# Performance work log

Measured on AMD Instinct MI355X. Metric: run time of the kernel, lower is better.

Reference implementation:

```python
import jax, jax.numpy as jnp
import numpy as np


def _c(x):
    # [2, ...] real/imag stacked -> complex
    return x[0] + 1j * x[1]


def _ri(z):
    # complex -> [2, ...] real/imag stacked
    return jnp.stack([jnp.real(z), jnp.imag(z)], axis=0).astype(jnp.float32)


_SHAPES = dict(
    VU=(2, 128, 96), UU=(2, 128, 8, 128), WU=(2, 8, 8, 128), GD=(2, 16, 96, 128),
    UD=(2, 16, 8, 128), WD=(2, 8, 8, 128), Z=(2, 16, 96, 128), HU=(2, 128, 16, 128),
    HD=(2, 16, 128, 128), P=(2, 16, 8, 128), GU=(2, 96, 16, 128), F=(2, 128, 8, 128),
    VD=(2, 96, 128), J=(2, 16, 16, 128, 128),
    conv1_w=(12, 18, 2, 2), conv1_b=(12,), conv2_w=(8, 12, 2, 2), conv2_b=(8,),
    conv3_w=(6, 8, 2, 2), conv3_b=(6,), fc1_w=(1000, 864), fc1_b=(1000,),
    fc2_w=(700, 1000), fc2_b=(700,), fc3_w=(192, 700), fc3_b=(192,))


def setup_inputs() -> dict:
    key = jax.random.key(0)
    keys = jax.random.split(key, len(_SHAPES))
    return {n: jax.random.normal(k, s, jnp.float32) * 0.05
            for (n, s), k in zip(_SHAPES.items(), keys)}


def reference(VU, UU, WU, GD, UD, WD, Z, HU, HD, P, GU, F, VD, J,
              conv1_w, conv1_b, conv2_w, conv2_b, conv3_w, conv3_b,
              fc1_w, fc1_b, fc2_w, fc2_b, fc3_w, fc3_b):
    VUc, UUc, WUc, GDc, UDc, WDc, Zc, HUc, HDc, Pc, GUc, Fc, VDc, Jc = map(
        _c, (VU, UU, WU, GD, UD, WD, Z, HU, HD, P, GU, F, VD, J))
    Mf = VUc.shape[1]

    # A1 = sum_k VU^H UU_k WU_k UU_k^H VU  (vectorized over k)
    T1 = jnp.einsum('nm,nuk->muk', jnp.conj(VUc), UUc)            # VU^H UU
    S1 = jnp.einsum('nvk,nf->vfk', jnp.conj(UUc), VUc)            # UU^H VU
    A1 = jnp.einsum('muk,uvk,vfk->mf', T1, WUc, S1)

    # A2 = sum_l GD_l^H UD_l WD_l UD_l^H GD_l
    T2 = jnp.einsum('nml,ndl->mdl', jnp.conj(GDc), UDc)           # GD^H UD
    S2 = jnp.einsum('ndl,nfl->dfl', jnp.conj(UDc), GDc)
    A2 = jnp.einsum('mdl,del,efl->mf', T2, WDc, S2)

    # A3 = sum_l Z_l^H UD_l WD_l UD_l^H Z_l
    T3 = jnp.einsum('nml,ndl->mdl', jnp.conj(Zc), UDc)            # Z^H UD
    S3 = jnp.einsum('ndl,nfl->dfl', jnp.conj(UDc), Zc)
    A3 = jnp.einsum('mdl,del,efl->mf', T3, WDc, S3)

    # B1 = B1_3 - B1_1 @ B1_2
    PPH = jnp.einsum('auk,buk->abk', Pc, jnp.conj(Pc))            # P P^H per k
    B1_1 = jnp.einsum('muk,uvk,nvk->mn', T1, WUc, jnp.conj(UUc))
    B1_2 = jnp.einsum('nak,abk,fbk->nf', HUc, PPH, jnp.conj(GUc))
    B1_3 = jnp.einsum('muk,vuk,avk,fak->mf', T1, jnp.conj(WUc), jnp.conj(Pc), jnp.conj(GUc))
    B1 = B1_3 - B1_1 @ B1_2

    # B2 = B2_3 - B2_1 @ B2_2
    FFH = jnp.einsum('adl,bdl->ab', Fc, jnp.conj(Fc))             # sum_l F F^H
    B2_1 = jnp.einsum('mdl,del,nel,ntl->mt', T2, WDc, jnp.conj(UDc), HDc)
    B2_2 = jnp.einsum('ab,fb->af', FFH, jnp.conj(VDc))
    B2_3 = jnp.einsum('mdl,edl,tel,ft->mf', T2, jnp.conj(WDc), jnp.conj(Fc), jnp.conj(VDc))
    B2 = B2_3 - B2_1 @ B2_2

    # B3 = -sum_{l,k} Z_l^H UD_l WD_l UD_l^H J_{kl} P_k P_k^H GU_k^H
    TL = jnp.einsum('mdl,del,nel->mnl', T3, WDc, jnp.conj(UDc))   # [Mf, N_D, L]
    Q = jnp.einsum('abk,fbk->afk', PPH, jnp.conj(GUc))            # [N_U, Mf, K]
    R = jnp.einsum('nakl,afk->nfl', Jc, Q)                        # sum over k
    B3 = -jnp.einsum('mnl,nfl->mf', TL, R)

    # C1 = C3 = sum_k GU_k P_k P_k^H GU_k^H ;  C2 = sum_l VD F_l F_l^H VD^H
    C1 = jnp.einsum('fak,abk,gbk->fg', GUc, PPH, jnp.conj(GUc))
    C2 = jnp.einsum('fa,ab,gb->fg', VDc, FFH, jnp.conj(VDc))
    C3 = C1

    # Theta_black_box CNN: cat nine [2,Mf,Mf] along channel -> [1,18,Mf,Mf]
    x = jnp.concatenate([_ri(M) for M in (A1, B1, C1, A2, B2, C2, A3, B3, C3)], axis=0)[None]
    for w, b in ((conv1_w, conv1_b), (conv2_w, conv2_b), (conv3_w, conv3_b)):
        x = jax.nn.relu(jax.lax.conv_general_dilated(
            x, w, (2, 2), 'VALID',
            dimension_numbers=('NCHW', 'OIHW', 'NCHW')) + b[None, :, None, None])
    x = x.reshape(-1, 864)
    x = jax.nn.relu(x @ fc1_w.T + fc1_b)
    x = jax.nn.relu(x @ fc2_w.T + fc2_b)
    x = jax.nn.relu(x @ fc3_w.T + fc3_b)
    return x.reshape(2, Mf)
```

## Files before the change

### kernel.cpp

```cpp
#include <hip/hip_runtime.h>

#define DEV __device__ __forceinline__

#define PL_VU 12288
#define PL_UU 131072
#define PL_WU 8192
#define PL_GD 196608
#define PL_UD 16384
#define PL_WD 8192
#define PL_Z  196608
#define PL_HU 262144
#define PL_HD 262144
#define PL_P  16384
#define PL_GU 196608
#define PL_F  131072
#define PL_VD 12288
#define PL_J  4194304

#define SP_T   98304
#define SP_PPH 32768
#define SP_Q   196608
#define SP_H2  262144

#define W_T1   0
#define W_T2   196608
#define W_T3   393216
#define W_PPH  589824
#define W_VF   655360
#define W_M1   851968
#define W_M1C  1048576
#define W_M2   1245184
#define W_M2C  1441792
#define W_M3   1638400
#define W_QT   1835008
#define W_G2   2228224
#define W_H2   2621440
#define W_U2   3145728
#define W_TL   3538944
#define W_N1   3932160
#define W_R    4325376
#define W_MATS 4718592
#define W_B11  4884480
#define W_B12  4909056
#define W_B21  4933632
#define W_B22  4958208
#define W_C1O  4982784
#define W_C2O  5010432
#define W_C3O  5015040
#define W_F1O  5015904
#define W_F2O  5016904

struct Ins {
  const float *VU,*UU,*WU,*GD,*UD,*WD,*Z,*HU,*HD,*P,*GU,*F,*VD,*J;
};

__global__ __launch_bounds__(256) void stageA(Ins in, float* __restrict__ ws) {
  int b = blockIdx.x, tid = threadIdx.x;
  if (b < 384) {
    int idx = b*256 + tid;
    int k = idx & 127, u = (idx >> 7) & 7, m = idx >> 10;
    float ar=0, ai=0;
    for (int n=0;n<128;++n) {
      float vr = in.VU[n*96+m], vi = in.VU[PL_VU+n*96+m];
      int iu = (n*8+u)*128+k;
      float ur = in.UU[iu], ui = in.UU[PL_UU+iu];
      ar += vr*ur + vi*ui; ai += vr*ui - vi*ur;
    }
    ws[W_T1+idx]=ar; ws[W_T1+SP_T+idx]=ai;
  } else if (b < 768) {
    int idx = (b-384)*256 + tid;
    int l = idx & 127, d = (idx >> 7) & 7, m = idx >> 10;
    float ar=0, ai=0;
    for (int n=0;n<16;++n) {
      int ig = (n*96+m)*128+l, iu = (n*8+d)*128+l;
      float gr = in.GD[ig], gi = in.GD[PL_GD+ig];
      float ur = in.UD[iu], ui = in.UD[PL_UD+iu];
      ar += gr*ur + gi*ui; ai += gr*ui - gi*ur;
    }
    ws[W_T2+idx]=ar; ws[W_T2+SP_T+idx]=ai;
  } else if (b < 1152) {
    int idx = (b-768)*256 + tid;
    int l = idx & 127, d = (idx >> 7) & 7, m = idx >> 10;
    float ar=0, ai=0;
    for (int n=0;n<16;++n) {
      int ig = (n*96+m)*128+l, iu = (n*8+d)*128+l;
      float gr = in.Z[ig], gi = in.Z[PL_Z+ig];
      float ur = in.UD[iu], ui = in.UD[PL_UD+iu];
      ar += gr*ur + gi*ui; ai += gr*ui - gi*ur;
    }
    ws[W_T3+idx]=ar; ws[W_T3+SP_T+idx]=ai;
  } else if (b < 1280) {
    int idx = (b-1152)*256 + tid;
    int k = idx & 127, bb = (idx >> 7) & 15, a = idx >> 11;
    float ar=0, ai=0;
    for (int u=0;u<8;++u) {
      int ia = (a*8+u)*128+k, ib = (bb*8+u)*128+k;
      float pr = in.P[ia], pi = in.P[PL_P+ia];
      float qr = in.P[ib], qi = in.P[PL_P+ib];
      ar += pr*qr + pi*qi; ai += pi*qr - pr*qi;
    }
    ws[W_PPH+idx]=ar; ws[W_PPH+SP_PPH+idx]=ai;
  } else {
    int idx = (b-1280)*256 + tid;
    int l = idx & 127, d = (idx >> 7) & 7, f = idx >> 10;
    float ar=0, ai=0;
    for (int a=0;a<128;++a) {
      float vr = in.VD[f*128+a], vi = in.VD[PL_VD+f*128+a];
      int ix = (a*8+d)*128+l;
      float fr = in.F[ix], fi = in.F[PL_F+ix];
      ar += vr*fr - vi*fi; ai += vr*fi + vi*fr;
    }
    ws[W_VF+idx]=ar; ws[W_VF+SP_T+idx]=ai;
  }
}

template<bool CONJA, bool CONJB, bool BENK, int N, int E>
DEV void inner_seg(const float* __restrict__ A, int Apl,
                   const float* __restrict__ B, int Bpl,
                   float* __restrict__ O, int Opl, int idx) {
  int k = idx & 127;
  int n = (idx >> 7) % N;
  int m = idx / (128*N);
  float ar=0, ai=0;
  #pragma unroll
  for (int e=0;e<E;++e) {
    int ia = (m*E+e)*128+k;
    float xr = A[ia], xi = A[Apl+ia];
    if (CONJA) xi = -xi;
    int ib = BENK ? (e*N+n)*128+k : (n*E+e)*128+k;
    float yr = B[ib], yi = B[Bpl+ib];
    if (CONJB) yi = -yi;
    ar += xr*yr - xi*yi; ai += xr*yi + xi*yr;
  }
  O[idx]=ar; O[Opl+idx]=ai;
}

__global__ __launch_bounds__(256) void stageB(Ins in, float* __restrict__ ws) {
  int b = blockIdx.x, tid = threadIdx.x;
  if (b < 384)       inner_seg<false,false,true ,8, 8>(ws+W_T1,SP_T, in.WU,PL_WU, ws+W_M1, SP_T, b*256+tid);
  else if (b < 768)  inner_seg<false,true ,false,8, 8>(ws+W_T1,SP_T, in.WU,PL_WU, ws+W_M1C,SP_T, (b-384)*256+tid);
  else if (b < 1152) inner_seg<false,false,true ,8, 8>(ws+W_T2,SP_T, in.WD,PL_WD, ws+W_M2, SP_T, (b-768)*256+tid);
  else if (b < 1536) inner_seg<false,true ,false,8, 8>(ws+W_T2,SP_T, in.WD,PL_WD, ws+W_M2C,SP_T, (b-1152)*256+tid);
  else if (b < 1920) inner_seg<false,false,true ,8, 8>(ws+W_T3,SP_T, in.WD,PL_WD, ws+W_M3, SP_T, (b-1536)*256+tid);
  else if (b < 2688) inner_seg<true ,false,false,16,16>(in.GU,PL_GU, ws+W_PPH,SP_PPH, ws+W_QT, SP_Q,  (b-1920)*256+tid);
  else if (b < 3456) inner_seg<false,true ,false,16,16>(in.GU,PL_GU, ws+W_PPH,SP_PPH, ws+W_G2, SP_Q,  (b-2688)*256+tid);
  else if (b < 4480) inner_seg<false,true ,false,16,16>(in.HU,PL_HU, ws+W_PPH,SP_PPH, ws+W_H2, SP_H2, (b-3456)*256+tid);
  else {
    int idx = (b-4480)*256 + tid;
    ((float4*)(ws+W_R))[idx] = make_float4(0.f,0.f,0.f,0.f);
  }
}

__global__ __launch_bounds__(256) void stageC(float* __restrict__ ws, Ins in) {
  int b = blockIdx.x, tid = threadIdx.x;
  if (b < 768)        inner_seg<false,true,false,16,8>(ws+W_M2, SP_T, in.UD,PL_UD, ws+W_U2, SP_Q, b*256+tid);
  else if (b < 1536)  inner_seg<false,true,false,16,8>(ws+W_M3, SP_T, in.UD,PL_UD, ws+W_TL, SP_Q, (b-768)*256+tid);
  else                inner_seg<false,true,false,16,8>(ws+W_M1C,SP_T, in.P, PL_P,  ws+W_N1, SP_Q, (b-1536)*256+tid);
}

__global__ __launch_bounds__(256) void kR(Ins in, float* __restrict__ ws) {
  int bid = blockIdx.x;
  int n  = bid >> 5;
  int lq = (bid >> 3) & 3;
  int kc = bid & 7;
  int tid = threadIdx.x;
  int l  = lq*32 + (tid & 31);
  int fs = tid >> 5;
  int k0 = kc*16;
  __shared__ float2 qt[96][16];
  float2 acc[12];
  #pragma unroll
  for (int j=0;j<12;++j) acc[j] = make_float2(0.f,0.f);
  for (int a=0;a<16;++a) {
    __syncthreads();
    for (int t=tid; t<96*16; t+=256) {
      int f = t >> 4, kk = t & 15;
      int qi = (f*16+a)*128 + k0 + kk;
      qt[f][kk] = make_float2(ws[W_QT+qi], ws[W_QT+SP_Q+qi]);
    }
    __syncthreads();
    const float* Jb = in.J + ((n*16+a)*128 + k0)*128 + l;
    #pragma unroll 4
    for (int kk=0;kk<16;++kk) {
      float jr = Jb[kk*128];
      float ji = Jb[PL_J + kk*128];
      #pragma unroll
      for (int j=0;j<12;++j) {
        float2 q = qt[fs*12+j][kk];
        acc[j].x += jr*q.x - ji*q.y;
        acc[j].y += jr*q.y + ji*q.x;
      }
    }
  }
  #pragma unroll
  for (int j=0;j<12;++j) {
    int f = fs*12+j;
    atomicAdd(&ws[W_R + (n*96+f)*128 + l], acc[j].x);
    atomicAdd(&ws[W_R + SP_Q + (n*96+f)*128 + l], acc[j].y);
  }
}

template<bool CONJB, bool OJC>
DEV void outer_tile(const float* __restrict__ A, int Apl,
                    const float* __restrict__ B, int Bpl,
                    float* __restrict__ C, int Cpl,
                    int J, int O, float scale, int tile) {
  __shared__ float As[16][33], Aip[16][33], Bs[16][33], Bip[16][33];
  int tj = J >> 4;
  int ti_ = tile / tj, tj_ = tile % tj;
  int tx = threadIdx.x & 15, ty = threadIdx.x >> 4;
  float ar=0, ai=0;
  int r0 = threadIdx.x >> 5, c = threadIdx.x & 31;
  for (int o=0;o<O;++o) {
    for (int cc=0;cc<128;cc+=32) {
      __syncthreads();
      #pragma unroll
      for (int rr=r0; rr<16; rr+=8) {
        int aidx = ((ti_*16+rr)*O+o)*128+cc+c;
        As[rr][c]=A[aidx]; Aip[rr][c]=A[Apl+aidx];
        int brow = tj_*16+rr;
        int bidx = OJC ? (o*J+brow)*128+cc+c : (brow*O+o)*128+cc+c;
        Bs[rr][c]=B[bidx]; Bip[rr][c]=B[Bpl+bidx];
      }
      __syncthreads();
      #pragma unroll
      for (int q=0;q<32;++q) {
        float xr=As[ty][q], xi=Aip[ty][q];
        float yr=Bs[tx][q], yi=Bip[tx][q];
        if (CONJB) { ar += xr*yr + xi*yi; ai += xi*yr - xr*yi; }
        else       { ar += xr*yr - xi*yi; ai += xr*yi + xi*yr; }
      }
    }
  }
  int i = ti_*16+ty, j = tj_*16+tx;
  C[i*J+j] = scale*ar; C[Cpl+i*J+j] = scale*ai;
}

__global__ __launch_bounds__(256) void stageD(Ins in, float* __restrict__ ws) {
  int b = blockIdx.x;
  if (b < 36)        outer_tile<true ,false>(ws+W_M1, SP_T,  ws+W_T1, SP_T,  ws+W_MATS+0*18432, 9216, 96, 8,  1.f, b);
  else if (b < 72)   outer_tile<true ,false>(ws+W_M2, SP_T,  ws+W_T2, SP_T,  ws+W_MATS+3*18432, 9216, 96, 8,  1.f, b-36);
  else if (b < 108)  outer_tile<true ,false>(ws+W_M3, SP_T,  ws+W_T3, SP_T,  ws+W_MATS+6*18432, 9216, 96, 8,  1.f, b-72);
  else if (b < 144)  outer_tile<true ,false>(ws+W_G2, SP_Q,  in.GU,   PL_GU, ws+W_MATS+2*18432, 9216, 96, 16, 1.f, b-108);
  else if (b < 180)  outer_tile<true ,false>(ws+W_G2, SP_Q,  in.GU,   PL_GU, ws+W_MATS+8*18432, 9216, 96, 16, 1.f, b-144);
  else if (b < 216)  outer_tile<true ,false>(ws+W_VF, SP_T,  ws+W_VF, SP_T,  ws+W_MATS+5*18432, 9216, 96, 8,  1.f, b-180);
  else if (b < 264)  outer_tile<true ,false>(ws+W_M1, SP_T,  in.UU,   PL_UU, ws+W_B11, 12288, 128, 8,  1.f, b-216);
  else if (b < 312)  outer_tile<true ,false>(ws+W_H2, SP_H2, in.GU,   PL_GU, ws+W_B12, 12288,  96, 16, 1.f, b-264);
  else if (b < 348)  outer_tile<true ,false>(ws+W_N1, SP_Q,  in.GU,   PL_GU, ws+W_MATS+1*18432, 9216, 96, 16, 1.f, b-312);
  else if (b < 396)  outer_tile<false,true >(ws+W_U2, SP_Q,  in.HD,   PL_HD, ws+W_B21, 12288, 128, 16, 1.f, b-348);
  else if (b < 444)  outer_tile<true ,false>(in.F,    PL_F,  ws+W_VF, SP_T,  ws+W_B22, 12288,  96, 8,  1.f, b-396);
  else if (b < 480)  outer_tile<true ,false>(ws+W_M2C,SP_T,  ws+W_VF, SP_T,  ws+W_MATS+4*18432, 9216, 96, 8,  1.f, b-444);
  else               outer_tile<false,true >(ws+W_TL, SP_Q,  ws+W_R,  SP_Q,  ws+W_MATS+7*18432, 9216, 96, 16,-1.f, b-480);
}

__global__ __launch_bounds__(256) void stageE(float* __restrict__ ws) {
  int idx = blockIdx.x*256 + threadIdx.x;
  int seg = idx / 9216;
  int t = idx % 9216;
  int m = t / 96, f = t % 96;
  const float* A = ws + (seg ? W_B21 : W_B11);
  const float* B = ws + (seg ? W_B22 : W_B12);
  float* C = ws + W_MATS + (seg ? 4 : 1)*18432;
  float ar = C[t], ai = C[9216+t];
  for (int n=0;n<128;++n) {
    float xr = A[m*128+n], xi = A[12288+m*128+n];
    float yr = B[n*96+f],  yi = B[12288+n*96+f];
    ar -= xr*yr - xi*yi;
    ai -= xr*yi + xi*yr;
  }
  C[t] = ar; C[9216+t] = ai;
}

__global__ __launch_bounds__(256) void convk(const float* __restrict__ x, const float* __restrict__ w,
                      const float* __restrict__ bias, float* __restrict__ out,
                      int IC, int IW, int OC, int OW) {
  int idx = blockIdx.x*256 + threadIdx.x;
  int total = OC*OW*OW;
  if (idx >= total) return;
  int ow = idx % OW, oh = (idx/OW) % OW, oc = idx/(OW*OW);
  float acc = bias[oc];
  const float* wk = w + oc*IC*4;
  for (int ic=0; ic<IC; ++ic) {
    const float* xp = x + ic*IW*IW + (oh*2)*IW + ow*2;
    acc += xp[0]*wk[0] + xp[1]*wk[1] + xp[IW]*wk[2] + xp[IW+1]*wk[3];
    wk += 4;
  }
  out[idx] = fmaxf(acc, 0.f);
}

__global__ __launch_bounds__(256) void fck(const float* __restrict__ W, const float* __restrict__ b,
                    const float* __restrict__ x, float* __restrict__ out,
                    int nout, int nin) {
  int wave = (blockIdx.x*256 + threadIdx.x) >> 6;
  int lane = threadIdx.x & 63;
  if (wave >= nout) return;
  float acc = 0.f;
  const float* Wr = W + (long)wave*nin;
  for (int c = lane; c < nin; c += 64) acc += Wr[c]*x[c];
  #pragma unroll
  for (int off=32; off; off>>=1) acc += __shfl_down(acc, off, 64);
  if (lane==0) out[wave] = fmaxf(acc + b[wave], 0.f);
}

extern "C" void kernel_launch(void* const* d_in, const int* in_sizes, int n_in,
                              void* d_out, int out_size, void* d_ws, size_t ws_size,
                              hipStream_t stream) {
  Ins in;
  in.VU=(const float*)d_in[0];  in.UU=(const float*)d_in[1];  in.WU=(const float*)d_in[2];
  in.GD=(const float*)d_in[3];  in.UD=(const float*)d_in[4];  in.WD=(const float*)d_in[5];
  in.Z =(const float*)d_in[6];  in.HU=(const float*)d_in[7];  in.HD=(const float*)d_in[8];
  in.P =(const float*)d_in[9];  in.GU=(const float*)d_in[10]; in.F =(const float*)d_in[11];
  in.VD=(const float*)d_in[12]; in.J =(const float*)d_in[13];
  float* ws = (float*)d_ws;

  stageA<<<1664,256, 0, stream>>>(in, ws);
  stageB<<<4864,256, 0, stream>>>(in, ws);
  stageC<<<2304,256, 0, stream>>>(ws, in);
  kR    <<<512, 256, 0, stream>>>(in, ws);
  stageD<<<516, 256, 0, stream>>>(in, ws);
  stageE<<<72,  256, 0, stream>>>(ws);
  convk <<<108, 256, 0, stream>>>(ws+W_MATS, (const float*)d_in[14], (const float*)d_in[15], ws+W_C1O, 18, 96, 12, 48);
  convk <<<18,  256, 0, stream>>>(ws+W_C1O,  (const float*)d_in[16], (const float*)d_in[17], ws+W_C2O, 12, 48, 8, 24);
  convk <<<4,   256, 0, stream>>>(ws+W_C2O,  (const float*)d_in[18], (const float*)d_in[19], ws+W_C3O, 8, 24, 6, 12);
  fck   <<<250, 256, 0, stream>>>((const float*)d_in[20], (const float*)d_in[21], ws+W_C3O, ws+W_F1O, 1000, 864);
  fck   <<<175, 256, 0, stream>>>((const float*)d_in[22], (const float*)d_in[23], ws+W_F1O, ws+W_F2O, 700, 1000);
  fck   <<<48,  256, 0, stream>>>((const float*)d_in[24], (const float*)d_in[25], ws+W_F2O, (float*)d_out, 192, 700);
}
```

Measured before the change: 498.2 us.

## Restructure kR with register-prefetched J tiles, 2 l per thread, split-a reduction

The J-contraction kernel now runs 256 blocks of 512 threads. Each thread handles two adjacent l columns through float2 loads. The two half-blocks each cover half of the a-range and are combined through shared memory before the atomics. J values for the next a are double-buffered in registers while the current one is computed, hiding global latency behind the FMA work. The larger register footprint (64 float2 of J plus 48 accumulators) risks lower occupancy or spills, and the grid has fewer blocks.

Result: slower. 1.179 ms (+136.6%).

```diff
diff --git a/kernel.cpp b/kernel.cpp
--- a/kernel.cpp
+++ b/kernel.cpp
@@ -158,46 +158,85 @@
   else                inner_seg<false,true,false,16,8>(ws+W_M1C,SP_T, in.P, PL_P,  ws+W_N1, SP_Q, (b-1536)*256+tid);
 }
 
-__global__ __launch_bounds__(256) void kR(Ins in, float* __restrict__ ws) {
+__global__ __launch_bounds__(512) void kR(Ins in, float* __restrict__ ws) {
   int bid = blockIdx.x;
-  int n  = bid >> 5;
-  int lq = (bid >> 3) & 3;
+  int n  = bid >> 4;
+  int lh = (bid >> 3) & 1;
   int kc = bid & 7;
   int tid = threadIdx.x;
-  int l  = lq*32 + (tid & 31);
-  int fs = tid >> 5;
-  int k0 = kc*16;
-  __shared__ float2 qt[96][16];
-  float2 acc[12];
+  int ah  = tid >> 8;
+  int g   = (tid >> 5) & 7;
+  int l0  = lh*64 + (tid & 31)*2;
+  int k0  = kc*16;
+
+  __shared__ float smem[12288];
+  float2* qt = (float2*)smem;
+
+  float accr[12][2], acci[12][2];
   #pragma unroll
-  for (int j=0;j<12;++j) acc[j] = make_float2(0.f,0.f);
-  for (int a=0;a<16;++a) {
+  for (int j=0;j<12;++j) { accr[j][0]=accr[j][1]=acci[j][0]=acci[j][1]=0.f; }
+
+  const float* Jbase = in.J + (n*16 + ah*8)*16384 + k0*128 + l0;
+  float2 jrA[16], jiA[16], jrB[16], jiB[16];
+
+#define LOADJ(R_, I_, rel) { const float* Jb = Jbase + (rel)*16384; \
+  _Pragma("unroll") for (int kk=0;kk<16;++kk) { \
+    R_[kk] = *(const float2*)(Jb + kk*128); \
+    I_[kk] = *(const float2*)(Jb + PL_J + kk*128); } }
+
+#define STAGE(iaa) { _Pragma("unroll") for (int t=tid; t<3072; t+=512) { \
+    int f = t >> 5, ahs = (t >> 4) & 1, kk = t & 15; \
+    int qi = (f*16 + ahs*8 + (iaa))*128 + k0 + kk; \
+    qt[t] = make_float2(ws[W_QT+qi], ws[W_QT+SP_Q+qi]); } }
+
+#define COMPUTE(R_, I_) { _Pragma("unroll") for (int kk=0;kk<16;++kk) { \
+    _Pragma("unroll") for (int j=0;j<12;++j) { \
+      float2 q = qt[((g*12+j)*2 + ah)*16 + kk]; \
+      accr[j][0] += R_[kk].x*q.x - I_[kk].x*q.y; \
+      acci[j][0] += R_[kk].x*q.y + I_[kk].x*q.x; \
+      accr[j][1] += R_[kk].y*q.x - I_[kk].y*q.y; \
+      acci[j][1] += R_[kk].y*q.y + I_[kk].y*q.x; } } }
+
+  LOADJ(jrA, jiA, 0)
+  #pragma unroll
+  for (int ia=0; ia<8; ia+=2) {
     __syncthreads();
-    for (int t=tid; t<96*16; t+=256) {
-      int f = t >> 4, kk = t & 15;
-      int qi = (f*16+a)*128 + k0 + kk;
-      qt[f][kk] = make_float2(ws[W_QT+qi], ws[W_QT+SP_Q+qi]);
-    }
+    STAGE(ia)
+    LOADJ(jrB, jiB, ia+1)
     __syncthreads();
-    const float* Jb = in.J + ((n*16+a)*128 + k0)*128 + l;
-    #pragma unroll 4
-    for (int kk=0;kk<16;++kk) {
-      float jr = Jb[kk*128];
-      float ji = Jb[PL_J + kk*128];
-      #pragma unroll
-      for (int j=0;j<12;++j) {
-        float2 q = qt[fs*12+j][kk];
-        acc[j].x += jr*q.x - ji*q.y;
-        acc[j].y += jr*q.y + ji*q.x;
-      }
-    }
-  }
-  #pragma unroll
-  for (int j=0;j<12;++j) {
-    int f = fs*12+j;
-    atomicAdd(&ws[W_R + (n*96+f)*128 + l], acc[j].x);
-    atomicAdd(&ws[W_R + SP_Q + (n*96+f)*128 + l], acc[j].y);
-  }
+    COMPUTE(jrA, jiA)
+    __syncthreads();
+    STAGE(ia+1)
+    if (ia+2 < 8) LOADJ(jrA, jiA, ia+2)
+    __syncthreads();
+    COMPUTE(jrB, jiB)
+  }
+
+  __syncthreads();
+  if (ah == 1) {
+    float* buf = smem + (tid-256)*48;
+    #pragma unroll
+    for (int j=0;j<12;++j) {
+      buf[j*4+0]=accr[j][0]; buf[j*4+1]=accr[j][1];
+      buf[j*4+2]=acci[j][0]; buf[j*4+3]=acci[j][1];
+    }
+  }
+  __syncthreads();
+  if (ah == 0) {
+    const float* buf = smem + tid*48;
+    #pragma unroll
+    for (int j=0;j<12;++j) {
+      int f = g*12+j;
+      int o = (n*96+f)*128 + l0;
+      atomicAdd(&ws[W_R + o],            accr[j][0] + buf[j*4+0]);
+      atomicAdd(&ws[W_R + o + 1],        accr[j][1] + buf[j*4+1]);
+      atomicAdd(&ws[W_R + SP_Q + o],     acci[j][0] + buf[j*4+2]);
+      atomicAdd(&ws[W_R + SP_Q + o + 1], acci[j][1] + buf[j*4+3]);
+    }
+  }
+#undef LOADJ
+#undef STAGE
+#undef COMPUTE
 }
 
 template<bool CONJB, bool OJC>
@@ -316,7 +355,7 @@
   stageA<<<1664,256, 0, stream>>>(in, ws);
   stageB<<<4864,256, 0, stream>>>(in, ws);
   stageC<<<2304,256, 0, stream>>>(ws, in);
-  kR    <<<512, 256, 0, stream>>>(in, ws);
+  kR    <<<256, 512, 0, stream>>>(in, ws);
   stageD<<<516, 256, 0, stream>>>(in, ws);
   stageE<<<72,  256, 0, stream>>>(ws);
   convk <<<108, 256, 0, stream>>>(ws+W_MATS, (const float*)d_in[14], (const float*)d_in[15], ws+W_C1O, 18, 96, 12, 48);
```

## Restructure kR with double-buffered Q staging, register-prefetched J and two columns per thread

Applied to the files above, without the earlier changes.

The J·Q reduction kernel now gives each thread two adjacent l columns, loaded as float2, and splits the a-loop across two blocks instead of splitting l into quarters. The Q tile is double-buffered in shared memory and J rows are prefetched into registers one half-step ahead, which removes one barrier per iteration and overlaps global loads with FMA work. The register footprint grows (48 accumulators plus the prefetched J values), and launch bounds ask for 2 blocks per CU. Splitting over a doubles the atomic traffic into R.

New measurement: 589.0 us. 18.2% more time.

```diff
diff --git a/kernel.cpp b/kernel.cpp
--- a/kernel.cpp
+++ b/kernel.cpp
@@ -158,46 +158,71 @@
   else                inner_seg<false,true,false,16,8>(ws+W_M1C,SP_T, in.P, PL_P,  ws+W_N1, SP_Q, (b-1536)*256+tid);
 }
 
-__global__ __launch_bounds__(256) void kR(Ins in, float* __restrict__ ws) {
+__global__ __launch_bounds__(256, 2) void kR(Ins in, float* __restrict__ ws) {
   int bid = blockIdx.x;
   int n  = bid >> 5;
-  int lq = (bid >> 3) & 3;
-  int kc = bid & 7;
+  int kc = (bid >> 2) & 7;
+  int lh = (bid >> 1) & 1;
+  int ah = bid & 1;
   int tid = threadIdx.x;
-  int l  = lq*32 + (tid & 31);
-  int fs = tid >> 5;
+  int g    = tid >> 5;
+  int lane = tid & 31;
+  int l0 = lh*64 + lane*2;
   int k0 = kc*16;
-  __shared__ float2 qt[96][16];
-  float2 acc[12];
+  int a0 = ah*8;
+
+  __shared__ float2 qt[2][1536];
+
+  float accr[12][2], acci[12][2];
   #pragma unroll
-  for (int j=0;j<12;++j) acc[j] = make_float2(0.f,0.f);
-  for (int a=0;a<16;++a) {
+  for (int j=0;j<12;++j) { accr[j][0]=accr[j][1]=acci[j][0]=acci[j][1]=0.f; }
+
+  const float* Jn = in.J + n*262144 + k0*128 + l0;
+  float2 jr0[8], ji0[8], jr1[8], ji1[8];
+
+#define LOADJ(JR, JI, a, h) { const float* Jb = Jn + (a)*16384 + (h)*1024; \
+  _Pragma("unroll") for (int kk=0;kk<8;++kk) { \
+    JR[kk] = *(const float2*)(Jb + kk*128); \
+    JI[kk] = *(const float2*)(Jb + PL_J + kk*128); } }
+
+#define STAGEQ(buf, a) { _Pragma("unroll") for (int i=0;i<6;++i) { \
+    int t = tid + i*256; int f = t >> 4, kk = t & 15; \
+    int qi = (f*16 + (a))*128 + k0 + kk; \
+    qt[buf][t] = make_float2(ws[W_QT+qi], ws[W_QT+SP_Q+qi]); } }
+
+#define COMPUTE(JR, JI, CUR, H) { _Pragma("unroll") for (int kk=0;kk<8;++kk) { \
+    _Pragma("unroll") for (int j=0;j<12;++j) { \
+      float2 q = qt[CUR][(g*12+j)*16 + (H)*8 + kk]; \
+      accr[j][0] += JR[kk].x*q.x - JI[kk].x*q.y; \
+      acci[j][0] += JR[kk].x*q.y + JI[kk].x*q.x; \
+      accr[j][1] += JR[kk].y*q.x - JI[kk].y*q.y; \
+      acci[j][1] += JR[kk].y*q.y + JI[kk].y*q.x; } } }
+
+  STAGEQ(0, a0)
+  LOADJ(jr0, ji0, a0, 0)
+  for (int ia=0; ia<8; ++ia) {
+    int a = a0 + ia;
+    int cur = ia & 1;
     __syncthreads();
-    for (int t=tid; t<96*16; t+=256) {
-      int f = t >> 4, kk = t & 15;
-      int qi = (f*16+a)*128 + k0 + kk;
-      qt[f][kk] = make_float2(ws[W_QT+qi], ws[W_QT+SP_Q+qi]);
-    }
-    __syncthreads();
-    const float* Jb = in.J + ((n*16+a)*128 + k0)*128 + l;
-    #pragma unroll 4
-    for (int kk=0;kk<16;++kk) {
-      float jr = Jb[kk*128];
-      float ji = Jb[PL_J + kk*128];
-      #pragma unroll
-      for (int j=0;j<12;++j) {
-        float2 q = qt[fs*12+j][kk];
-        acc[j].x += jr*q.x - ji*q.y;
-        acc[j].y += jr*q.y + ji*q.x;
-      }
-    }
-  }
+    LOADJ(jr1, ji1, a, 1)
+    if (ia < 7) STAGEQ(cur^1, a+1)
+    COMPUTE(jr0, ji0, cur, 0)
+    if (ia < 7) LOADJ(jr0, ji0, a+1, 0)
+    COMPUTE(jr1, ji1, cur, 1)
+  }
+
   #pragma unroll
   for (int j=0;j<12;++j) {
-    int f = fs*12+j;
-    atomicAdd(&ws[W_R + (n*96+f)*128 + l], acc[j].x);
-    atomicAdd(&ws[W_R + SP_Q + (n*96+f)*128 + l], acc[j].y);
-  }
+    int f = g*12+j;
+    int o = (n*96+f)*128 + l0;
+    atomicAdd(&ws[W_R + o],            accr[j][0]);
+    atomicAdd(&ws[W_R + o + 1],        accr[j][1]);
+    atomicAdd(&ws[W_R + SP_Q + o],     acci[j][0]);
+    atomicAdd(&ws[W_R + SP_Q + o + 1], acci[j][1]);
+  }
+#undef LOADJ
+#undef STAGEQ
+#undef COMPUTE
 }
 
 template<bool CONJB, bool OJC>
```
